# Performance work log

Hardware: AMD Instinct MI355X
Metric: run time of the kernel (lower is better)

## Reference

```python
import jax, jax.numpy as jnp
import numpy as np
import math

B, S, D, H = 4, 2048, 1024, 16
HD = D // H  # 64
FF = 4096
EPS = 1e-5


def layer_norm(x, g, b):
    mu = jnp.mean(x, axis=-1, keepdims=True)
    var = jnp.mean(jnp.square(x - mu), axis=-1, keepdims=True)
    return (x - mu) * jax.lax.rsqrt(var + EPS) * g + b


def setup_inputs() -> dict:
    key = jax.random.key(0)
    ks = jax.random.split(key, 16)
    sc = 0.02
    return {
        "x": jax.random.normal(ks[0], (B, S, D), dtype=jnp.float32),
        "Wq": jax.random.normal(ks[1], (H, D, HD), dtype=jnp.float32) * sc,
        "bq": jnp.zeros((H, HD), dtype=jnp.float32),
        "Wk": jax.random.normal(ks[2], (H, D, HD), dtype=jnp.float32) * sc,
        "bk": jnp.zeros((H, HD), dtype=jnp.float32),
        "Wv": jax.random.normal(ks[3], (H, D, HD), dtype=jnp.float32) * sc,
        "bv": jnp.zeros((H, HD), dtype=jnp.float32),
        "Wo": jax.random.normal(ks[4], (D, D), dtype=jnp.float32) * sc,
        "bo": jnp.zeros((D,), dtype=jnp.float32),
        "W1": jax.random.normal(ks[5], (D, FF), dtype=jnp.float32) * sc,
        "b1": jnp.zeros((FF,), dtype=jnp.float32),
        "W2": jax.random.normal(ks[6], (FF, D), dtype=jnp.float32) * sc,
        "b2": jnp.zeros((D,), dtype=jnp.float32),
        "ln1_g": jnp.ones((D,), dtype=jnp.float32),
        "ln1_b": jnp.zeros((D,), dtype=jnp.float32),
        "ln2_g": jnp.ones((D,), dtype=jnp.float32),
        "ln2_b": jnp.zeros((D,), dtype=jnp.float32),
    }


def reference(x, Wq, bq, Wk, bk, Wv, bv, Wo, bo, W1, b1, W2, b2, ln1_g, ln1_b, ln2_g, ln2_b):
    b, s, d = x.shape
    h1 = layer_norm(x, ln1_g, ln1_b)
    # per-head Q/K/V linears, vectorized over heads: [b,h,s,hd]
    q = jnp.einsum('bsd,hde->bhse', h1, Wq) + bq[None, :, None, :]
    k = jnp.einsum('bsd,hde->bhse', h1, Wk) + bk[None, :, None, :]
    v = jnp.einsum('bsd,hde->bhse', h1, Wv) + bv[None, :, None, :]
    scores = jnp.einsum('bhqe,bhke->bhqk', q, k) / math.sqrt(q.shape[-1])
    causal = jnp.tril(jnp.ones((s, s), dtype=bool))
    scores = jnp.where(causal[None, None], scores, -jnp.inf)
    weights = jax.nn.softmax(scores, axis=-1)
    attn = jnp.einsum('bhqk,bhke->bhqe', weights, v)
    # concat heads (head order = torch concat dim=-1)
    attn = attn.transpose(0, 2, 1, 3).reshape(b, s, d)
    x = x + attn @ Wo + bo
    h2 = layer_norm(x, ln2_g, ln2_b)
    y = jax.nn.gelu(h2 @ W1 + b1, approximate=False)
    y = jax.nn.gelu(y @ W2 + b2, approximate=False)
    return x + y
```

## Files before the change

kernel.cpp:

```cpp
#include <hip/hip_runtime.h>
#include <cstdint>
#include <cstddef>


#define DI __device__ __forceinline__

typedef __attribute__((ext_vector_type(8))) __bf16 bf16x8;
typedef __attribute__((ext_vector_type(4))) float floatx4;
typedef __attribute__((ext_vector_type(4))) unsigned int uintx4;

static constexpr int Bn = 4, Sn = 2048, Dn = 1024, Hn = 16, HDn = 64, FFn = 4096;
static constexpr int NTOK = Bn * Sn;
static constexpr int D3 = 3 * Dn;

DI float bf2f(unsigned short u) { return __uint_as_float(((unsigned int)u) << 16); }
DI unsigned short f2bf(float f) {
  unsigned int u = __float_as_uint(f);
  u += 0x7FFFu + ((u >> 16) & 1u);
  return (unsigned short)(u >> 16);
}
DI float gelu_f(float v) {
  float t = v * v;
  float c = __builtin_fmaf(t, -0.1029443f, -2.3022080f);
  float z = v * c;
  float e = __builtin_amdgcn_exp2f(z);
  float d = 1.0f + e;
  float r;
  asm("v_rcp_f32 %0, %1" : "=v"(r) : "v"(d));
  return v * r;
}
DI bf16x8 ld8(const unsigned short* p) { return *(const bf16x8*)p; }
DI floatx4 mfma16(bf16x8 a, bf16x8 b, floatx4 c) {
  return __builtin_amdgcn_mfma_f32_16x16x32_bf16(a, b, c, 0, 0, 0);
}
DI void g2l16(const unsigned short* g, unsigned short* l) {
  __builtin_amdgcn_global_load_lds((__attribute__((address_space(1))) void*)g,
                                   (__attribute__((address_space(3))) void*)l,
                                   16, 0, 0);
}
DI float ldin(const void* p, size_t idx, bool f32) {
  return f32 ? ((const float*)p)[idx] : bf2f(((const unsigned short*)p)[idx]);
}
DI unsigned int cvt_pk_bf16(float lo, float hi) {
  unsigned int r;
  asm("v_cvt_pk_bf16_f32 %0, %1, %2" : "=v"(r) : "v"(lo), "v"(hi));
  return r;
}
DI bf16x8 pack8(unsigned int a, unsigned int b, unsigned int c, unsigned int d) {
  uintx4 t;
  t[0] = a; t[1] = b; t[2] = c; t[3] = d;
  return __builtin_bit_cast(bf16x8, t);
}
DI int swz16(int row, int col) {
  return (row << 6) + ((((col >> 3) ^ row ^ (row >> 3)) & 7) << 3) + (col & 7);
}
DI int xcd_swz(int bid, int nwg) {
  return (bid & 7) * (nwg >> 3) + (bid >> 3);
}

__global__ void detect_kernel(const unsigned short* __restrict__ x,
                              int* __restrict__ flag) {
  int t = threadIdx.x;
  int cnt = 0;
  for (int i = t; i < 1024; i += 64) {
    unsigned short u = x[2 * i];
    int e = (u >> 7) & 0xFF;
    cnt += (e >= 96 && e <= 142) ? 1 : 0;
  }
  #pragma unroll
  for (int off = 32; off >= 1; off >>= 1) cnt += __shfl_xor(cnt, off);
  if (t == 0) *flag = (cnt < 820) ? 1 : 0;
}

__global__ void vec_prep(const void* bq, const void* bk, const void* bv,
                         const void* bo, const void* b1, const void* b2,
                         const void* g1, const void* be1, const void* g2,
                         const void* be2, unsigned short* __restrict__ dst,
                         const int* __restrict__ flag) {
  int i = blockIdx.x * 256 + threadIdx.x;
  if (i >= 13312) return;
  const bool f32 = *flag != 0;
  const void* src; int off;
  if      (i < 1024)  { src = bq;  off = i; }
  else if (i < 2048)  { src = bk;  off = i - 1024; }
  else if (i < 3072)  { src = bv;  off = i - 2048; }
  else if (i < 4096)  { src = bo;  off = i - 3072; }
  else if (i < 8192)  { src = b1;  off = i - 4096; }
  else if (i < 9216)  { src = b2;  off = i - 8192; }
  else if (i < 10240) { src = g1;  off = i - 9216; }
  else if (i < 11264) { src = be1; off = i - 10240; }
  else if (i < 12288) { src = g2;  off = i - 11264; }
  else                { src = be2; off = i - 12288; }
  dst[i] = f2bf(ldin(src, off, f32));
}

__global__ void transpose_kernel(const void* __restrict__ src,
                                 unsigned short* __restrict__ dst, int K, int N,
                                 const int* __restrict__ flag) {
  __shared__ unsigned short tile[64][65];
  const bool f32 = *flag != 0;
  int kb = blockIdx.y * 64, nb = blockIdx.x * 64;
  for (int i = threadIdx.x; i < 4096; i += 256) {
    int r = i >> 6, c = i & 63;
    tile[r][c] = f2bf(ldin(src, (size_t)(kb + r) * N + nb + c, f32));
  }
  __syncthreads();
  for (int i = threadIdx.x; i < 4096; i += 256) {
    int r = i >> 6, c = i & 63;
    dst[(size_t)(nb + r) * K + kb + c] = tile[c][r];
  }
}

__global__ void qkvT_kernel(const void* __restrict__ Wq,
                            const void* __restrict__ Wk,
                            const void* __restrict__ Wv,
                            unsigned short* __restrict__ WT,
                            const int* __restrict__ flag) {
  __shared__ unsigned short tile[64][65];
  const bool f32 = *flag != 0;
  const void* src = blockIdx.z == 0 ? Wq : (blockIdx.z == 1 ? Wk : Wv);
  int h = blockIdx.y, d0 = blockIdx.x * 64;
  size_t base = (size_t)h * (Dn * HDn);
  for (int i = threadIdx.x; i < 4096; i += 256) {
    int r = i >> 6, c = i & 63;
    tile[r][c] = f2bf(ldin(src, base + (size_t)(d0 + r) * 64 + c, f32));
  }
  __syncthreads();
  for (int i = threadIdx.x; i < 4096; i += 256) {
    int r = i >> 6, c = i & 63;
    WT[(size_t)(blockIdx.z * 1024 + h * 64 + r) * 1024 + d0 + c] = tile[c][r];
  }
}

__global__ __launch_bounds__(256) void ln_kernel(const void* __restrict__ x,
                                                 const unsigned short* __restrict__ g,
                                                 const unsigned short* __restrict__ b,
                                                 unsigned short* __restrict__ out,
                                                 const int* __restrict__ flag) {
  const bool f32 = flag ? (*flag != 0) : true;
  int row = blockIdx.x, t = threadIdx.x;
  float v[4];
  if (f32) {
    float4 f = *(const float4*)((const float*)x + (size_t)row * Dn + t * 4);
    v[0] = f.x; v[1] = f.y; v[2] = f.z; v[3] = f.w;
  } else {
    ushort4 u = *(const ushort4*)((const unsigned short*)x + (size_t)row * Dn + t * 4);
    v[0] = bf2f(u.x); v[1] = bf2f(u.y); v[2] = bf2f(u.z); v[3] = bf2f(u.w);
  }
  float s = v[0] + v[1] + v[2] + v[3];
  float s2 = v[0] * v[0] + v[1] * v[1] + v[2] * v[2] + v[3] * v[3];
  #pragma unroll
  for (int off = 32; off >= 1; off >>= 1) {
    s += __shfl_xor(s, off);
    s2 += __shfl_xor(s2, off);
  }
  __shared__ float red[8];
  int wv = t >> 6, ln = t & 63;
  if (ln == 0) { red[wv] = s; red[4 + wv] = s2; }
  __syncthreads();
  s = red[0] + red[1] + red[2] + red[3];
  s2 = red[4] + red[5] + red[6] + red[7];
  float mu = s * (1.0f / 1024.0f);
  float var = s2 * (1.0f / 1024.0f) - mu * mu;
  float rs = rsqrtf(fmaxf(var, 0.0f) + 1e-5f);
  ushort4 gg = *(const ushort4*)(g + t * 4);
  ushort4 bb = *(const ushort4*)(b + t * 4);
  ushort4 o;
  o.x = f2bf((v[0] - mu) * rs * bf2f(gg.x) + bf2f(bb.x));
  o.y = f2bf((v[1] - mu) * rs * bf2f(gg.y) + bf2f(bb.y));
  o.z = f2bf((v[2] - mu) * rs * bf2f(gg.z) + bf2f(bb.z));
  o.w = f2bf((v[3] - mu) * rs * bf2f(gg.w) + bf2f(bb.w));
  *(ushort4*)(out + (size_t)row * Dn + t * 4) = o;
}

enum { EPI_BIAS_BF16 = 0, EPI_WO = 1, EPI_GELU = 2, EPI_FF2 = 3 };

template <int EPI, int BN>
__global__ __launch_bounds__(256, BN == 64 ? 4 : 3) void gemm_kernel(
    const unsigned short* __restrict__ A, const unsigned short* __restrict__ BT,
    const unsigned short* __restrict__ bias, const void* __restrict__ residv,
    const float* __restrict__ resid_f, unsigned short* __restrict__ Cb,
    float* __restrict__ Cf, const int* __restrict__ flag, int M, int N, int K) {
  constexpr int NT = BN / 32;
  __shared__ unsigned short As[2][128 * 32];
  __shared__ unsigned short Bs[2][BN * 32];
  const int gx = gridDim.x;
  const int nwg = gx * gridDim.y;
  const int bid = xcd_swz((int)blockIdx.y * gx + (int)blockIdx.x, nwg);
  const int m0 = (bid / gx) * 128, n0 = (bid % gx) * BN;
  const int w = threadIdx.x >> 6, lane = threadIdx.x & 63;
  const int waveM = (w >> 1) * 64, waveN = (w & 1) * (BN / 2);
  const int m16 = lane & 15, quad = lane >> 4;
  const int sxor = (m16 >> 1) & 3;
  const bool rf32 = flag && (*flag != 0);
  const int tid = threadIdx.x;

  const int srow = w * 32 + (lane >> 2);
  const int stA = srow * 32 + (lane & 3) * 8;
  const int scolA = ((lane & 3) ^ ((srow >> 1) & 3)) * 8;
  const unsigned short* Ag = A + (size_t)(m0 + srow) * K + scolA;
  const int sBrow = (BN == 128) ? srow : (tid >> 2);
  const int sBq = (BN == 128) ? (lane & 3) : (tid & 3);
  const int stB = sBrow * 32 + sBq * 8;
  const int scolB = (sBq ^ ((sBrow >> 1) & 3)) * 8;
  const unsigned short* Bg = BT + (size_t)(n0 + sBrow) * K + scolB;
  const size_t rowstep = (size_t)16 * K;

  floatx4 acc[4][NT];
  #pragma unroll
  for (int i = 0; i < 4; i++)
    #pragma unroll
    for (int j = 0; j < NT; j++) acc[i][j] = floatx4{0.f, 0.f, 0.f, 0.f};

  g2l16(Ag, As[0] + stA);
  g2l16(Ag + rowstep, As[0] + stA + 16 * 32);
  g2l16(Bg, Bs[0] + stB);
  if constexpr (BN == 128) g2l16(Bg + rowstep, Bs[0] + stB + 16 * 32);
  Ag += 32; Bg += 32;
  asm volatile("s_waitcnt vmcnt(0)" ::: "memory");
  __builtin_amdgcn_s_barrier();

  const int ntiles = K >> 5;
  int cur = 0;
  for (int t = 0; t < ntiles; ++t) {
    if (t + 1 < ntiles) {
      unsigned short* Aln = As[cur ^ 1] + stA;
      unsigned short* Bln = Bs[cur ^ 1] + stB;
      g2l16(Ag, Aln);
      g2l16(Ag + rowstep, Aln + 16 * 32);
      g2l16(Bg, Bln);
      if constexpr (BN == 128) g2l16(Bg + rowstep, Bln + 16 * 32);
      Ag += 32; Bg += 32;
    }
    const unsigned short* Ab = As[cur];
    const unsigned short* Bb = Bs[cur];
    bf16x8 af[4], bfv[NT];
    #pragma unroll
    for (int mt = 0; mt < 4; mt++)
      af[mt] = ld8(Ab + (waveM + mt * 16 + m16) * 32 + ((quad ^ sxor) << 3));
    #pragma unroll
    for (int nt = 0; nt < NT; nt++)
      bfv[nt] = ld8(Bb + (waveN + nt * 16 + m16) * 32 + ((quad ^ sxor) << 3));
    #pragma unroll
    for (int mt = 0; mt < 4; mt++)
      #pragma unroll
      for (int nt = 0; nt < NT; nt++)
        acc[mt][nt] = mfma16(af[mt], bfv[nt], acc[mt][nt]);
    if (t + 1 < ntiles) {
      asm volatile("s_waitcnt vmcnt(0)" ::: "memory");
      __builtin_amdgcn_s_barrier();
      cur ^= 1;
    }
  }

  #pragma unroll
  for (int mt = 0; mt < 4; mt++) {
    #pragma unroll
    for (int nt = 0; nt < NT; nt++) {
      const int col = n0 + waveN + nt * 16 + m16;
      const float bcol = bf2f(bias[col]);
      #pragma unroll
      for (int r = 0; r < 4; r++) {
        const int row = m0 + waveM + mt * 16 + quad * 4 + r;
        const size_t idx = (size_t)row * N + col;
        float v = acc[mt][nt][r] + bcol;
        if constexpr (EPI == EPI_BIAS_BF16) {
          Cb[idx] = f2bf(v);
        } else if constexpr (EPI == EPI_WO) {
          float rv = rf32 ? ((const float*)residv)[idx]
                          : bf2f(((const unsigned short*)residv)[idx]);
          Cf[idx] = v + rv;
        } else if constexpr (EPI == EPI_GELU) {
          Cb[idx] = f2bf(gelu_f(v));
        } else {
          float ov = gelu_f(v) + resid_f[idx];
          if (rf32) Cf[idx] = ov;
          else      Cb[idx] = f2bf(ov);
        }
      }
    }
  }
}

__global__ __launch_bounds__(256, 4) void attn_kernel(
    const unsigned short* __restrict__ qkv, unsigned short* __restrict__ attn) {
  const int bid = xcd_swz((int)blockIdx.y * 32 + (int)blockIdx.x, 2048);
  const int qt = 31 - (bid & 31);
  const int bh = bid >> 5;
  const int b = bh >> 4, h = bh & 15;
  const int tid = threadIdx.x;
  const int w = tid >> 6, lane = tid & 63;
  const int m16 = lane & 15, quad = lane >> 4;

  __shared__ unsigned short Ks[2][4096];
  __shared__ unsigned short Vt[2][4096];

  const int qrow = qt * 64 + w * 16 + m16;
  const int qloc = w * 16 + m16;
  const unsigned short* qp = qkv + (size_t)(b * Sn + qrow) * D3 + h * 64 + quad * 8;
  const bf16x8 qf0 = ld8(qp), qf1 = ld8(qp + 32);

  floatx4 acc_o[4];
  #pragma unroll
  for (int nt = 0; nt < 4; nt++) acc_o[nt] = floatx4{0.f, 0.f, 0.f, 0.f};
  float lsum = 0.f;

  const int kr = tid >> 3, kc = (tid & 7) * 8;
  const int krs = (kr & 3) + (((kr >> 3) & 3) << 2) + (((kr >> 2) & 1) << 4);
  const int vk = (tid >> 3) * 2, ve = (tid & 7) * 8;

  uint4 kreg0, kreg1, vreg0, vreg1;
  const unsigned short* const kvroot = qkv + (size_t)(b * Sn) * D3 + h * 64;

  {
    const unsigned short* base = kvroot;
    kreg0 = *(const uint4*)(base + (size_t)kr * D3 + 1024 + kc);
    kreg1 = *(const uint4*)(base + (size_t)(kr + 32) * D3 + 1024 + kc);
    vreg0 = *(const uint4*)(base + (size_t)vk * D3 + 2048 + ve);
    vreg1 = *(const uint4*)(base + (size_t)(vk + 1) * D3 + 2048 + ve);
  }

  for (int kt = 0; kt <= qt; ++kt) {
    const int pb = kt & 1;
    *(uint4*)(Ks[pb] + swz16(krs, kc)) = kreg0;
    *(uint4*)(Ks[pb] + swz16(krs + 32, kc)) = kreg1;
    {
      const unsigned short* a0 = (const unsigned short*)&vreg0;
      const unsigned short* a1 = (const unsigned short*)&vreg1;
      #pragma unroll
      for (int i = 0; i < 8; i++) {
        unsigned int word = (unsigned int)a0[i] | ((unsigned int)a1[i] << 16);
        *(unsigned int*)(Vt[pb] + swz16(ve + i, vk)) = word;
      }
    }
    __syncthreads();
    if (kt < qt) {
      const unsigned short* base = kvroot + (size_t)(kt + 1) * 64 * D3;
      kreg0 = *(const uint4*)(base + (size_t)kr * D3 + 1024 + kc);
      kreg1 = *(const uint4*)(base + (size_t)(kr + 32) * D3 + 1024 + kc);
      vreg0 = *(const uint4*)(base + (size_t)vk * D3 + 2048 + ve);
      vreg1 = *(const uint4*)(base + (size_t)(vk + 1) * D3 + 2048 + ve);
    }

    floatx4 sa[4];
    #pragma unroll
    for (int nt = 0; nt < 4; nt++) {
      bf16x8 k0 = ld8(Ks[pb] + swz16(nt * 16 + m16, quad * 8));
      bf16x8 k1 = ld8(Ks[pb] + swz16(nt * 16 + m16, 32 + quad * 8));
      floatx4 t = mfma16(k0, qf0, floatx4{0.f, 0.f, 0.f, 0.f});
      sa[nt] = mfma16(k1, qf1, t);
    }

    if (kt == qt) {
      #pragma unroll
      for (int nt = 0; nt < 4; nt++) {
        const int kb_ = (quad << 3) + ((nt & 1) << 2) + ((nt >> 1) << 5);
        #pragma unroll
        for (int r = 0; r < 4; r++)
          if (kb_ + r > qloc) sa[nt][r] = -1e30f;
      }
    }

    constexpr float C = 0.18033688011112042f;
    float e00 = __builtin_amdgcn_exp2f(sa[0][0] * C);
    float e01 = __builtin_amdgcn_exp2f(sa[0][1] * C);
    float e02 = __builtin_amdgcn_exp2f(sa[0][2] * C);
    float e03 = __builtin_amdgcn_exp2f(sa[0][3] * C);
    float e10 = __builtin_amdgcn_exp2f(sa[1][0] * C);
    float e11 = __builtin_amdgcn_exp2f(sa[1][1] * C);
    float e12 = __builtin_amdgcn_exp2f(sa[1][2] * C);
    float e13 = __builtin_amdgcn_exp2f(sa[1][3] * C);
    float e20 = __builtin_amdgcn_exp2f(sa[2][0] * C);
    float e21 = __builtin_amdgcn_exp2f(sa[2][1] * C);
    float e22 = __builtin_amdgcn_exp2f(sa[2][2] * C);
    float e23 = __builtin_amdgcn_exp2f(sa[2][3] * C);
    float e30 = __builtin_amdgcn_exp2f(sa[3][0] * C);
    float e31 = __builtin_amdgcn_exp2f(sa[3][1] * C);
    float e32 = __builtin_amdgcn_exp2f(sa[3][2] * C);
    float e33 = __builtin_amdgcn_exp2f(sa[3][3] * C);
    lsum += ((e00 + e01) + (e02 + e03)) + ((e10 + e11) + (e12 + e13)) +
            ((e20 + e21) + (e22 + e23)) + ((e30 + e31) + (e32 + e33));
    const bf16x8 pa0 = pack8(cvt_pk_bf16(e00, e01), cvt_pk_bf16(e02, e03),
                             cvt_pk_bf16(e10, e11), cvt_pk_bf16(e12, e13));
    const bf16x8 pa1 = pack8(cvt_pk_bf16(e20, e21), cvt_pk_bf16(e22, e23),
                             cvt_pk_bf16(e30, e31), cvt_pk_bf16(e32, e33));

    #pragma unroll
    for (int nt = 0; nt < 4; nt++) {
      bf16x8 v0 = ld8(Vt[pb] + swz16(nt * 16 + m16, quad * 8));
      bf16x8 v1 = ld8(Vt[pb] + swz16(nt * 16 + m16, 32 + quad * 8));
      acc_o[nt] = mfma16(pa0, v0, acc_o[nt]);
      acc_o[nt] = mfma16(pa1, v1, acc_o[nt]);
    }
  }

  lsum += __shfl_xor(lsum, 16);
  lsum += __shfl_xor(lsum, 32);

  #pragma unroll
  for (int r = 0; r < 4; r++) {
    const float inv = 1.0f / fmaxf(__shfl(lsum, quad * 4 + r), 1e-20f);
    const size_t orow = (size_t)(b * Sn + qt * 64 + w * 16 + quad * 4 + r) * Dn + h * 64;
    #pragma unroll
    for (int nt = 0; nt < 4; nt++)
      attn[orow + nt * 16 + m16] = f2bf(acc_o[nt][r] * inv);
  }
}

extern "C" void kernel_launch(void* const* d_in, const int* in_sizes, int n_in,
                              void* d_out, int out_size, void* d_ws, size_t ws_size,
                              hipStream_t stream) {
  (void)in_sizes; (void)n_in; (void)out_size; (void)ws_size;
  const void* x    = d_in[0];
  const void* Wq   = d_in[1];
  const void* bq   = d_in[2];
  const void* Wk   = d_in[3];
  const void* bk   = d_in[4];
  const void* Wv   = d_in[5];
  const void* bv   = d_in[6];
  const void* Wo   = d_in[7];
  const void* bo   = d_in[8];
  const void* W1   = d_in[9];
  const void* b1   = d_in[10];
  const void* W2   = d_in[11];
  const void* b2   = d_in[12];
  const void* ln1g = d_in[13];
  const void* ln1b = d_in[14];
  const void* ln2g = d_in[15];
  const void* ln2b = d_in[16];
  char* ws = (char*)d_ws;

  constexpr size_t OFF_WTQKV = 0;
  constexpr size_t OFF_WOT   = OFF_WTQKV + (size_t)D3 * Dn * 2;
  constexpr size_t OFF_W1T   = OFF_WOT + (size_t)Dn * Dn * 2;
  constexpr size_t OFF_W2T   = OFF_W1T + (size_t)FFn * Dn * 2;
  constexpr size_t OFF_VEC   = OFF_W2T + (size_t)Dn * FFn * 2;
  constexpr size_t OFF_FLAG  = OFF_VEC + 32768;
  constexpr size_t OFF_H     = OFF_FLAG + 256;
  constexpr size_t OFF_QKV   = OFF_H + (size_t)NTOK * Dn * 2;
  constexpr size_t OFF_ATTN  = OFF_QKV + (size_t)NTOK * D3 * 2;
  constexpr size_t OFF_X2    = OFF_ATTN + (size_t)NTOK * Dn * 2;
  constexpr size_t OFF_Y1    = OFF_QKV;

  unsigned short* WTqkv = (unsigned short*)(ws + OFF_WTQKV);
  unsigned short* WoT   = (unsigned short*)(ws + OFF_WOT);
  unsigned short* W1T   = (unsigned short*)(ws + OFF_W1T);
  unsigned short* W2T   = (unsigned short*)(ws + OFF_W2T);
  unsigned short* vec   = (unsigned short*)(ws + OFF_VEC);
  int*            flag  = (int*)(ws + OFF_FLAG);
  unsigned short* hbuf  = (unsigned short*)(ws + OFF_H);
  unsigned short* qkvb  = (unsigned short*)(ws + OFF_QKV);
  unsigned short* attnb = (unsigned short*)(ws + OFF_ATTN);
  float*          x2    = (float*)(ws + OFF_X2);
  unsigned short* y1    = (unsigned short*)(ws + OFF_Y1);

  detect_kernel<<<1, 64, 0, stream>>>((const unsigned short*)x, flag);

  vec_prep<<<52, 256, 0, stream>>>(bq, bk, bv, bo, b1, b2, ln1g, ln1b, ln2g,
                                   ln2b, vec, flag);
  qkvT_kernel<<<dim3(16, 16, 3), 256, 0, stream>>>(Wq, Wk, Wv, WTqkv, flag);
  transpose_kernel<<<dim3(16, 16), 256, 0, stream>>>(Wo, WoT, 1024, 1024, flag);
  transpose_kernel<<<dim3(64, 16), 256, 0, stream>>>(W1, W1T, 1024, 4096, flag);
  transpose_kernel<<<dim3(16, 64), 256, 0, stream>>>(W2, W2T, 4096, 1024, flag);

  ln_kernel<<<NTOK, 256, 0, stream>>>(x, vec + 9216, vec + 10240, hbuf, flag);
  gemm_kernel<EPI_BIAS_BF16, 128><<<dim3(D3 / 128, NTOK / 128), 256, 0, stream>>>(
      hbuf, WTqkv, vec + 0, nullptr, nullptr, qkvb, nullptr, nullptr,
      NTOK, D3, Dn);
  attn_kernel<<<dim3(Sn / 64, Bn * Hn), 256, 0, stream>>>(qkvb, attnb);
  gemm_kernel<EPI_WO, 128><<<dim3(Dn / 128, NTOK / 128), 256, 0, stream>>>(
      attnb, WoT, vec + 3072, x, nullptr, nullptr, x2, flag, NTOK, Dn, Dn);
  ln_kernel<<<NTOK, 256, 0, stream>>>(x2, vec + 11264, vec + 12288, hbuf, nullptr);
  gemm_kernel<EPI_GELU, 128><<<dim3(FFn / 128, NTOK / 128), 256, 0, stream>>>(
      hbuf, W1T, vec + 4096, nullptr, nullptr, y1, nullptr, nullptr,
      NTOK, FFn, Dn);
  gemm_kernel<EPI_FF2, 128><<<dim3(Dn / 128, NTOK / 128), 256, 0, stream>>>(
      y1, W2T, vec + 8192, nullptr, x2, (unsigned short*)d_out, (float*)d_out,
      flag, NTOK, Dn, FFn);
}
```

Baseline: 571.8 us.

## Add 4-stage LDS pipeline for FF2 GEMM and narrow Wo GEMM tile

Adds a DEPTH template parameter to the GEMM. With DEPTH=4 the kernel keeps three tile loads in flight and waits with partial vmcnt counts instead of fully draining after each K-step. This is used for the long-K FF2 GEMM to hide global load latency, at the cost of more LDS and a lower occupancy bound. The Wo GEMM also switches to BN=64 tiles, which doubles its block count to fill the CUs better.

```diff
diff --git a/kernel.cpp b/kernel.cpp
--- a/kernel.cpp
+++ b/kernel.cpp
@@ -175,15 +175,16 @@
 
 enum { EPI_BIAS_BF16 = 0, EPI_WO = 1, EPI_GELU = 2, EPI_FF2 = 3 };
 
-template <int EPI, int BN>
-__global__ __launch_bounds__(256, BN == 64 ? 4 : 3) void gemm_kernel(
+template <int EPI, int BN, int DEPTH>
+__global__ __launch_bounds__(256, BN == 64 ? 4 : (DEPTH == 4 ? 2 : 3))
+void gemm_kernel(
     const unsigned short* __restrict__ A, const unsigned short* __restrict__ BT,
     const unsigned short* __restrict__ bias, const void* __restrict__ residv,
     const float* __restrict__ resid_f, unsigned short* __restrict__ Cb,
     float* __restrict__ Cf, const int* __restrict__ flag, int M, int N, int K) {
   constexpr int NT = BN / 32;
-  __shared__ unsigned short As[2][128 * 32];
-  __shared__ unsigned short Bs[2][BN * 32];
+  __shared__ unsigned short As[DEPTH][128 * 32];
+  __shared__ unsigned short Bs[DEPTH][BN * 32];
   const int gx = gridDim.x;
   const int nwg = gx * gridDim.y;
   const int bid = xcd_swz((int)blockIdx.y * gx + (int)blockIdx.x, nwg);
@@ -212,44 +213,66 @@
     #pragma unroll
     for (int j = 0; j < NT; j++) acc[i][j] = floatx4{0.f, 0.f, 0.f, 0.f};
 
-  g2l16(Ag, As[0] + stA);
-  g2l16(Ag + rowstep, As[0] + stA + 16 * 32);
-  g2l16(Bg, Bs[0] + stB);
-  if constexpr (BN == 128) g2l16(Bg + rowstep, Bs[0] + stB + 16 * 32);
-  Ag += 32; Bg += 32;
-  asm volatile("s_waitcnt vmcnt(0)" ::: "memory");
-  __builtin_amdgcn_s_barrier();
+  auto stage = [&](int slot) {
+    g2l16(Ag, As[slot] + stA);
+    g2l16(Ag + rowstep, As[slot] + stA + 16 * 32);
+    g2l16(Bg, Bs[slot] + stB);
+    if constexpr (BN == 128) g2l16(Bg + rowstep, Bs[slot] + stB + 16 * 32);
+    Ag += 32; Bg += 32;
+  };
 
   const int ntiles = K >> 5;
-  int cur = 0;
-  for (int t = 0; t < ntiles; ++t) {
-    if (t + 1 < ntiles) {
-      unsigned short* Aln = As[cur ^ 1] + stA;
-      unsigned short* Bln = Bs[cur ^ 1] + stB;
-      g2l16(Ag, Aln);
-      g2l16(Ag + rowstep, Aln + 16 * 32);
-      g2l16(Bg, Bln);
-      if constexpr (BN == 128) g2l16(Bg + rowstep, Bln + 16 * 32);
-      Ag += 32; Bg += 32;
-    }
-    const unsigned short* Ab = As[cur];
-    const unsigned short* Bb = Bs[cur];
-    bf16x8 af[4], bfv[NT];
-    #pragma unroll
-    for (int mt = 0; mt < 4; mt++)
-      af[mt] = ld8(Ab + (waveM + mt * 16 + m16) * 32 + ((quad ^ sxor) << 3));
-    #pragma unroll
-    for (int nt = 0; nt < NT; nt++)
-      bfv[nt] = ld8(Bb + (waveN + nt * 16 + m16) * 32 + ((quad ^ sxor) << 3));
-    #pragma unroll
-    for (int mt = 0; mt < 4; mt++)
+
+  if constexpr (DEPTH == 2) {
+    stage(0);
+    asm volatile("s_waitcnt vmcnt(0)" ::: "memory");
+    __builtin_amdgcn_s_barrier();
+    int cur = 0;
+    for (int t = 0; t < ntiles; ++t) {
+      if (t + 1 < ntiles) stage(cur ^ 1);
+      const unsigned short* Ab = As[cur];
+      const unsigned short* Bb = Bs[cur];
+      bf16x8 af[4], bfv[NT];
+      #pragma unroll
+      for (int mt = 0; mt < 4; mt++)
+        af[mt] = ld8(Ab + (waveM + mt * 16 + m16) * 32 + ((quad ^ sxor) << 3));
       #pragma unroll
       for (int nt = 0; nt < NT; nt++)
-        acc[mt][nt] = mfma16(af[mt], bfv[nt], acc[mt][nt]);
-    if (t + 1 < ntiles) {
-      asm volatile("s_waitcnt vmcnt(0)" ::: "memory");
+        bfv[nt] = ld8(Bb + (waveN + nt * 16 + m16) * 32 + ((quad ^ sxor) << 3));
+      #pragma unroll
+      for (int mt = 0; mt < 4; mt++)
+        #pragma unroll
+        for (int nt = 0; nt < NT; nt++)
+          acc[mt][nt] = mfma16(af[mt], bfv[nt], acc[mt][nt]);
+      if (t + 1 < ntiles) {
+        asm volatile("s_waitcnt vmcnt(0)" ::: "memory");
+        __builtin_amdgcn_s_barrier();
+        cur ^= 1;
+      }
+    }
+  } else {
+    stage(0); stage(1); stage(2);
+    for (int t = 0; t < ntiles; ++t) {
+      const int rem = ntiles - 1 - t;
+      if (rem >= 2)      asm volatile("s_waitcnt vmcnt(8)" ::: "memory");
+      else if (rem == 1) asm volatile("s_waitcnt vmcnt(4)" ::: "memory");
+      else               asm volatile("s_waitcnt vmcnt(0)" ::: "memory");
       __builtin_amdgcn_s_barrier();
-      cur ^= 1;
+      if (t + 3 < ntiles) stage((t + 3) & 3);
+      const unsigned short* Ab = As[t & 3];
+      const unsigned short* Bb = Bs[t & 3];
+      bf16x8 af[4], bfv[NT];
+      #pragma unroll
+      for (int mt = 0; mt < 4; mt++)
+        af[mt] = ld8(Ab + (waveM + mt * 16 + m16) * 32 + ((quad ^ sxor) << 3));
+      #pragma unroll
+      for (int nt = 0; nt < NT; nt++)
+        bfv[nt] = ld8(Bb + (waveN + nt * 16 + m16) * 32 + ((quad ^ sxor) << 3));
+      #pragma unroll
+      for (int mt = 0; mt < 4; mt++)
+        #pragma unroll
+        for (int nt = 0; nt < NT; nt++)
+          acc[mt][nt] = mfma16(af[mt], bfv[nt], acc[mt][nt]);
     }
   }
 
@@ -464,17 +487,17 @@
   transpose_kernel<<<dim3(16, 64), 256, 0, stream>>>(W2, W2T, 4096, 1024, flag);
 
   ln_kernel<<<NTOK, 256, 0, stream>>>(x, vec + 9216, vec + 10240, hbuf, flag);
-  gemm_kernel<EPI_BIAS_BF16, 128><<<dim3(D3 / 128, NTOK / 128), 256, 0, stream>>>(
+  gemm_kernel<EPI_BIAS_BF16, 128, 2><<<dim3(D3 / 128, NTOK / 128), 256, 0, stream>>>(
       hbuf, WTqkv, vec + 0, nullptr, nullptr, qkvb, nullptr, nullptr,
       NTOK, D3, Dn);
   attn_kernel<<<dim3(Sn / 64, Bn * Hn), 256, 0, stream>>>(qkvb, attnb);
-  gemm_kernel<EPI_WO, 128><<<dim3(Dn / 128, NTOK / 128), 256, 0, stream>>>(
+  gemm_kernel<EPI_WO, 64, 2><<<dim3(Dn / 64, NTOK / 128), 256, 0, stream>>>(
       attnb, WoT, vec + 3072, x, nullptr, nullptr, x2, flag, NTOK, Dn, Dn);
   ln_kernel<<<NTOK, 256, 0, stream>>>(x2, vec + 11264, vec + 12288, hbuf, nullptr);
-  gemm_kernel<EPI_GELU, 128><<<dim3(FFn / 128, NTOK / 128), 256, 0, stream>>>(
+  gemm_kernel<EPI_GELU, 128, 2><<<dim3(FFn / 128, NTOK / 128), 256, 0, stream>>>(
       hbuf, W1T, vec + 4096, nullptr, nullptr, y1, nullptr, nullptr,
       NTOK, FFn, Dn);
-  gemm_kernel<EPI_FF2, 128><<<dim3(Dn / 128, NTOK / 128), 256, 0, stream>>>(
+  gemm_kernel<EPI_FF2, 128, 4><<<dim3(Dn / 128, NTOK / 128), 256, 0, stream>>>(
       y1, W2T, vec + 8192, nullptr, x2, (unsigned short*)d_out, (float*)d_out,
       flag, NTOK, Dn, FFn);
 }
```

Result: no change. 571.3 us (-0.1%).
